# Kernel optimization log

Measured on AMD Instinct MI355X. Metric: run time of the kernel, lower is better.

The kernel has to match this reference:

```python
import jax, jax.numpy as jnp
import numpy as np

LATENT = 1024
ENC = 4096
B = 8192


def setup_inputs() -> dict:
    key = jax.random.key(0)
    k1, k2, k3, k4 = jax.random.split(key, 4)
    inp = jax.random.normal(k1, (B, LATENT), dtype=jnp.float32)
    enc = jax.random.normal(k2, (B, ENC), dtype=jnp.float32)
    # nn.Linear(ENC, LATENT): weight [LATENT, ENC], bias [LATENT]
    bound = 1.0 / np.sqrt(ENC)
    W = jax.random.uniform(k3, (LATENT, ENC), minval=-bound, maxval=bound, dtype=jnp.float32)
    b = jax.random.uniform(k4, (LATENT,), minval=-bound, maxval=bound, dtype=jnp.float32)
    return {"input": inp, "encoder_output": enc, "W": W, "b": b}


def reference(input, encoder_output, W, b):
    # vector = Linear(encoder_output)  -> [B, LATENT]
    v = jnp.einsum("be,de->bd", encoder_output, W) + b
    # Fused Householder-style reflection (math identical to bmm(vv^T, x)):
    # out = x - 2 * v * (v . x) / ||v||   (original divides by norm, not norm^2)
    dot = jnp.sum(v * input, axis=1, keepdims=True)          # [B, 1]
    norm = jnp.linalg.norm(v, axis=1, keepdims=True)         # [B, 1]
    output = input - 2.0 * v * dot / norm                    # [B, LATENT]
    log_det = jnp.zeros((input.shape[0], 1), dtype=input.dtype)
    return (output, log_det)
```

## Files before the change

### kernel.cpp

```cpp
#include <hip/hip_runtime.h>
#include <hip/hip_bf16.h>
#include <stdint.h>

#define M_DIM 8192
#define N_DIM 1024
#define K_DIM 4096

typedef __bf16 bf16x8 __attribute__((ext_vector_type(8)));
typedef float f32x4 __attribute__((ext_vector_type(4)));
typedef __hip_bfloat16 bf16_t;

__device__ __forceinline__ void gload_lds16(const void* g, void* l) {
  __builtin_amdgcn_global_load_lds(
      (const __attribute__((address_space(1))) void*)g,
      (__attribute__((address_space(3))) void*)l, 16, 0, 0);
}

__global__ __launch_bounds__(256) void pack_both(const float* __restrict__ enc,
                                                 const float* __restrict__ W,
                                                 int4* __restrict__ pA,
                                                 int4* __restrict__ pB) {
  const unsigned gtid = blockIdx.x * 256 + threadIdx.x;
  const float* src;
  int4* dst;
  unsigned t;
  if (gtid < 4194304u) { src = enc; dst = pA; t = gtid; }
  else                 { src = W;   dst = pB; t = gtid - 4194304u; }
  const unsigned cp = t & 7;
  const unsigned tmp = t >> 3;
  const unsigned r = tmp & 255;
  const unsigned tmp2 = tmp >> 8;
  const unsigned kt = tmp2 & 63;
  const unsigned rt = tmp2 >> 6;
  const unsigned srow = (rt << 8) + r;
  const unsigned k0 = (kt << 6) + ((cp ^ (r & 7)) << 3);
  const float4* s = (const float4*)(src + (size_t)srow * 4096 + k0);
  float4 a = s[0], b = s[1];
  union { bf16_t h[8]; int4 v; } u;
  u.h[0] = __float2bfloat16(a.x); u.h[1] = __float2bfloat16(a.y);
  u.h[2] = __float2bfloat16(a.z); u.h[3] = __float2bfloat16(a.w);
  u.h[4] = __float2bfloat16(b.x); u.h[5] = __float2bfloat16(b.y);
  u.h[6] = __float2bfloat16(b.z); u.h[7] = __float2bfloat16(b.w);
  dst[t] = u.v;
}

__device__ __forceinline__ void stage_half(const char* g, char* smem, int ldsoff, int tid) {
  gload_lds16(g + tid * 16, smem + ldsoff + tid * 16);
  gload_lds16(g + 8192 + tid * 16, smem + ldsoff + 8192 + tid * 16);
}

__global__ __launch_bounds__(512, 2) void gemm8(
    const char* __restrict__ pA, const char* __restrict__ pB,
    float* __restrict__ V0, float* __restrict__ V1p, int NT) {
  extern __shared__ char smem[];
  const int tid = threadIdx.x;
  const int lane = tid & 63, wave = tid >> 6;
  const int wm = wave >> 2, wn = wave & 3;
  const int lrow = lane & 15, lkc = lane >> 4;

  const int cpx = (int)gridDim.x >> 3;
  const int swz = ((int)blockIdx.x & 7) * cpx + ((int)blockIdx.x >> 3);
  const int split = swz >> 7;
  const int rem = swz & 127;
  const int mt = rem >> 2, nt = rem & 3;

  const char* Abase = pA + ((size_t)mt * 64 + (size_t)split * NT) * 32768;
  const char* Bbase = pB + ((size_t)nt * 64 + (size_t)split * NT) * 32768;
  float* V = split ? V1p : V0;

  int colw[2];
  colw[0] = ((lkc) ^ (lrow & 7)) << 4;
  colw[1] = ((4 + lkc) ^ (lrow & 7)) << 4;
  int aRow[4], bRow[2];
  #pragma unroll
  for (int f = 0; f < 4; ++f) aRow[f] = (wm * 64 + f * 16 + lrow) * 128;
  #pragma unroll
  for (int f2 = 0; f2 < 2; ++f2) bRow[f2] = 32768 + (wn * 32 + f2 * 16 + lrow) * 128;

  f32x4 acc[2][4][2][2];
  #pragma unroll
  for (int a0 = 0; a0 < 2; ++a0)
    #pragma unroll
    for (int a1 = 0; a1 < 4; ++a1)
      #pragma unroll
      for (int a2 = 0; a2 < 2; ++a2)
        #pragma unroll
        for (int a3 = 0; a3 < 2; ++a3)
          acc[a0][a1][a2][a3] = (f32x4){0.f, 0.f, 0.f, 0.f};

  const int ktm = NT - 1;

  stage_half(Abase,         smem, 0, tid);
  stage_half(Bbase,         smem, 32768, tid);
  stage_half(Bbase + 16384, smem, 49152, tid);
  stage_half(Abase + 16384, smem, 16384, tid);
  stage_half(Abase + 32768, smem, 65536, tid);
  asm volatile("s_waitcnt vmcnt(4)" ::: "memory");
  __builtin_amdgcn_sched_barrier(0);
  __builtin_amdgcn_s_barrier();

  bf16x8 aE[4][2], aO[4][2], b0[2][2], b1[2][2];
  #pragma unroll
  for (int f = 0; f < 4; ++f)
    #pragma unroll
    for (int s = 0; s < 2; ++s)
      aE[f][s] = *(const bf16x8*)(smem + aRow[f] + colw[s]);
  #pragma unroll
  for (int f2 = 0; f2 < 2; ++f2)
    #pragma unroll
    for (int s = 0; s < 2; ++s)
      b0[f2][s] = *(const bf16x8*)(smem + bRow[f2] + colw[s]);

  for (int g = 0; g < NT; ++g) {
    const int bb = g & 1, nbf = bb ^ 1;
    char* ab = smem + bb * 65536;
    char* nb = smem + nbf * 65536;
    const char* A1t = Abase + (size_t)((g + 1) & ktm) * 32768;
    const char* B1t = Bbase + (size_t)((g + 1) & ktm) * 32768;
    const char* A2t = Abase + (size_t)((g + 2) & ktm) * 32768;

    #pragma unroll
    for (int f2 = 0; f2 < 2; ++f2)
      #pragma unroll
      for (int s = 0; s < 2; ++s)
        b1[f2][s] = *(const bf16x8*)(ab + bRow[f2] + 16384 + colw[s]);
    stage_half(B1t, smem, nbf * 65536 + 32768, tid);
    stage_half(B1t + 16384, smem, nbf * 65536 + 49152, tid);
    __builtin_amdgcn_s_setprio(1);
    #pragma unroll
    for (int f = 0; f < 4; ++f)
      #pragma unroll
      for (int f2 = 0; f2 < 2; ++f2)
        #pragma unroll
        for (int s = 0; s < 2; ++s)
          acc[0][f][0][f2] = __builtin_amdgcn_mfma_f32_16x16x32_bf16(
              aE[f][s], b0[f2][s], acc[0][f][0][f2], 0, 0, 0);
    __builtin_amdgcn_s_setprio(0);
    asm volatile("s_waitcnt vmcnt(6)" ::: "memory");
    __builtin_amdgcn_sched_barrier(0);
    __builtin_amdgcn_s_barrier();

    #pragma unroll
    for (int f = 0; f < 4; ++f)
      #pragma unroll
      for (int s = 0; s < 2; ++s)
        aO[f][s] = *(const bf16x8*)(ab + aRow[f] + 16384 + colw[s]);
    stage_half(A1t + 16384, smem, nbf * 65536 + 16384, tid);
    __builtin_amdgcn_s_setprio(1);
    #pragma unroll
    for (int f = 0; f < 4; ++f)
      #pragma unroll
      for (int f2 = 0; f2 < 2; ++f2)
        #pragma unroll
        for (int s = 0; s < 2; ++s)
          acc[0][f][1][f2] = __builtin_amdgcn_mfma_f32_16x16x32_bf16(
              aE[f][s], b1[f2][s], acc[0][f][1][f2], 0, 0, 0);
    __builtin_amdgcn_s_setprio(0);
    __builtin_amdgcn_sched_barrier(0);
    __builtin_amdgcn_s_barrier();

    stage_half(A2t, smem, bb * 65536, tid);
    __builtin_amdgcn_s_setprio(1);
    #pragma unroll
    for (int f = 0; f < 4; ++f)
      #pragma unroll
      for (int f2 = 0; f2 < 2; ++f2)
        #pragma unroll
        for (int s = 0; s < 2; ++s)
          acc[1][f][1][f2] = __builtin_amdgcn_mfma_f32_16x16x32_bf16(
              aO[f][s], b1[f2][s], acc[1][f][1][f2], 0, 0, 0);
    __builtin_amdgcn_s_setprio(0);
    asm volatile("s_waitcnt vmcnt(8)" ::: "memory");
    __builtin_amdgcn_sched_barrier(0);
    __builtin_amdgcn_s_barrier();

    #pragma unroll
    for (int f = 0; f < 4; ++f)
      #pragma unroll
      for (int s = 0; s < 2; ++s)
        aE[f][s] = *(const bf16x8*)(nb + aRow[f] + colw[s]);
    __builtin_amdgcn_s_setprio(1);
    #pragma unroll
    for (int f = 0; f < 4; ++f)
      #pragma unroll
      for (int f2 = 0; f2 < 2; ++f2)
        #pragma unroll
        for (int s = 0; s < 2; ++s)
          acc[1][f][0][f2] = __builtin_amdgcn_mfma_f32_16x16x32_bf16(
              aO[f][s], b0[f2][s], acc[1][f][0][f2], 0, 0, 0);
    __builtin_amdgcn_s_setprio(0);
    __builtin_amdgcn_sched_barrier(0);
    asm volatile("s_waitcnt vmcnt(4)" ::: "memory");
    #pragma unroll
    for (int f2 = 0; f2 < 2; ++f2)
      #pragma unroll
      for (int s = 0; s < 2; ++s)
        b0[f2][s] = *(const bf16x8*)(nb + bRow[f2] + colw[s]);
    __builtin_amdgcn_sched_barrier(0);
    __builtin_amdgcn_s_barrier();
  }

  const int lq = lane >> 4;
  #pragma unroll
  for (int qm = 0; qm < 2; ++qm)
    #pragma unroll
    for (int f = 0; f < 4; ++f) {
      const int rowg = mt * 256 + qm * 128 + wm * 64 + f * 16 + lq * 4;
      #pragma unroll
      for (int reg = 0; reg < 4; ++reg) {
        float* Vr = V + (size_t)(rowg + reg) * N_DIM + nt * 256 + wn * 32 + lrow;
        #pragma unroll
        for (int qn = 0; qn < 2; ++qn)
          #pragma unroll
          for (int f2 = 0; f2 < 2; ++f2)
            Vr[qn * 128 + f2 * 16] = acc[qm][f][qn][f2][reg];
      }
    }
}

__global__ __launch_bounds__(256) void householder_ep(
    const float* __restrict__ x, const float* __restrict__ bias,
    float* __restrict__ vio, const float* __restrict__ V2,
    float* __restrict__ logdet) {
  const int row = blockIdx.x;
  const int t = threadIdx.x;
  float4* vr = (float4*)(vio + (size_t)row * N_DIM);
  const float4* xr = (const float4*)(x + (size_t)row * N_DIM);
  const float4* br = (const float4*)bias;

  float4 v = vr[t];
  if (V2) {
    float4 v2 = ((const float4*)(V2 + (size_t)row * N_DIM))[t];
    v.x += v2.x; v.y += v2.y; v.z += v2.z; v.w += v2.w;
  }
  float4 bb = br[t];
  v.x += bb.x; v.y += bb.y; v.z += bb.z; v.w += bb.w;
  float4 xx = xr[t];

  float dot = v.x * xx.x + v.y * xx.y + v.z * xx.z + v.w * xx.w;
  float nsq = v.x * v.x + v.y * v.y + v.z * v.z + v.w * v.w;

  #pragma unroll
  for (int off = 32; off > 0; off >>= 1) {
    dot += __shfl_down(dot, off);
    nsq += __shfl_down(nsq, off);
  }
  __shared__ float sd[4], sn[4];
  if ((t & 63) == 0) { sd[t >> 6] = dot; sn[t >> 6] = nsq; }
  __syncthreads();
  dot = sd[0] + sd[1] + sd[2] + sd[3];
  nsq = sn[0] + sn[1] + sn[2] + sn[3];

  const float f = 2.0f * dot / sqrtf(nsq);
  float4 o;
  o.x = xx.x - f * v.x;
  o.y = xx.y - f * v.y;
  o.z = xx.z - f * v.z;
  o.w = xx.w - f * v.w;
  vr[t] = o;
  if (t == 0) logdet[row] = 0.0f;
}

extern "C" void kernel_launch(void* const* d_in, const int* in_sizes, int n_in,
                              void* d_out, int out_size, void* d_ws, size_t ws_size,
                              hipStream_t stream) {
  const float* x   = (const float*)d_in[0];
  const float* enc = (const float*)d_in[1];
  const float* W   = (const float*)d_in[2];
  const float* b   = (const float*)d_in[3];

  float* out    = (float*)d_out;
  float* v      = out;
  float* logdet = out + (size_t)M_DIM * N_DIM;

  char*  packA = (char*)d_ws;
  char*  packB = packA + (size_t)64 * 1024 * 1024;
  float* V2    = (float*)(packB + (size_t)8 * 1024 * 1024);

  const size_t need2 = (size_t)104 * 1024 * 1024;
  const int nsplit = (ws_size >= need2) ? 2 : 1;

  pack_both<<<18432, 256, 0, stream>>>(enc, W, (int4*)packA, (int4*)packB);

  hipFuncSetAttribute((const void*)gemm8, hipFuncAttributeMaxDynamicSharedMemorySize, 131072);
  gemm8<<<dim3(128 * nsplit), 512, 131072, stream>>>(
      packA, packB, v, nsplit == 2 ? V2 : nullptr, 64 / nsplit);

  householder_ep<<<M_DIM, 256, 0, stream>>>(x, b, v, nsplit == 2 ? V2 : nullptr, logdet);
}
```

Baseline: 118.8 us.

## Store GEMM partials as bf16 and move LDS reads after MFMA blocks

The split-K GEMM partial results are now written to workspace as bf16 instead of fp32, and the epilogue reads and widens them. This halves the intermediate write and read traffic between the GEMM and the Householder epilogue, but rounding the partial sums to bf16 adds error to v. The LDS fragment loads for b1, aO and aE are also moved to after each MFMA group, before the barrier, so they overlap differently with matrix compute.

```diff
diff --git a/kernel.cpp b/kernel.cpp
--- a/kernel.cpp
+++ b/kernel.cpp
@@ -14,6 +14,12 @@
   __builtin_amdgcn_global_load_lds(
       (const __attribute__((address_space(1))) void*)g,
       (__attribute__((address_space(3))) void*)l, 16, 0, 0);
+}
+
+__device__ __forceinline__ float b2f(unsigned short u) {
+  union { unsigned i; float f; } x;
+  x.i = ((unsigned)u) << 16;
+  return x.f;
 }
 
 __global__ __launch_bounds__(256) void pack_both(const float* __restrict__ enc,
@@ -51,7 +57,7 @@
 
 __global__ __launch_bounds__(512, 2) void gemm8(
     const char* __restrict__ pA, const char* __restrict__ pB,
-    float* __restrict__ V0, float* __restrict__ V1p, int NT) {
+    bf16_t* __restrict__ V0, bf16_t* __restrict__ V1p, int NT) {
   extern __shared__ char smem[];
   const int tid = threadIdx.x;
   const int lane = tid & 63, wave = tid >> 6;
@@ -66,7 +72,7 @@
 
   const char* Abase = pA + ((size_t)mt * 64 + (size_t)split * NT) * 32768;
   const char* Bbase = pB + ((size_t)nt * 64 + (size_t)split * NT) * 32768;
-  float* V = split ? V1p : V0;
+  bf16_t* V = split ? V1p : V0;
 
   int colw[2];
   colw[0] = ((lkc) ^ (lrow & 7)) << 4;
@@ -119,11 +125,6 @@
     const char* B1t = Bbase + (size_t)((g + 1) & ktm) * 32768;
     const char* A2t = Abase + (size_t)((g + 2) & ktm) * 32768;
 
-    #pragma unroll
-    for (int f2 = 0; f2 < 2; ++f2)
-      #pragma unroll
-      for (int s = 0; s < 2; ++s)
-        b1[f2][s] = *(const bf16x8*)(ab + bRow[f2] + 16384 + colw[s]);
     stage_half(B1t, smem, nbf * 65536 + 32768, tid);
     stage_half(B1t + 16384, smem, nbf * 65536 + 49152, tid);
     __builtin_amdgcn_s_setprio(1);
@@ -136,15 +137,16 @@
           acc[0][f][0][f2] = __builtin_amdgcn_mfma_f32_16x16x32_bf16(
               aE[f][s], b0[f2][s], acc[0][f][0][f2], 0, 0, 0);
     __builtin_amdgcn_s_setprio(0);
+    __builtin_amdgcn_sched_barrier(0);
+    #pragma unroll
+    for (int f2 = 0; f2 < 2; ++f2)
+      #pragma unroll
+      for (int s = 0; s < 2; ++s)
+        b1[f2][s] = *(const bf16x8*)(ab + bRow[f2] + 16384 + colw[s]);
     asm volatile("s_waitcnt vmcnt(6)" ::: "memory");
     __builtin_amdgcn_sched_barrier(0);
     __builtin_amdgcn_s_barrier();
 
-    #pragma unroll
-    for (int f = 0; f < 4; ++f)
-      #pragma unroll
-      for (int s = 0; s < 2; ++s)
-        aO[f][s] = *(const bf16x8*)(ab + aRow[f] + 16384 + colw[s]);
     stage_half(A1t + 16384, smem, nbf * 65536 + 16384, tid);
     __builtin_amdgcn_s_setprio(1);
     #pragma unroll
@@ -157,6 +159,12 @@
               aE[f][s], b1[f2][s], acc[0][f][1][f2], 0, 0, 0);
     __builtin_amdgcn_s_setprio(0);
     __builtin_amdgcn_sched_barrier(0);
+    #pragma unroll
+    for (int f = 0; f < 4; ++f)
+      #pragma unroll
+      for (int s = 0; s < 2; ++s)
+        aO[f][s] = *(const bf16x8*)(ab + aRow[f] + 16384 + colw[s]);
+    __builtin_amdgcn_sched_barrier(0);
     __builtin_amdgcn_s_barrier();
 
     stage_half(A2t, smem, bb * 65536, tid);
@@ -170,15 +178,16 @@
           acc[1][f][1][f2] = __builtin_amdgcn_mfma_f32_16x16x32_bf16(
               aO[f][s], b1[f2][s], acc[1][f][1][f2], 0, 0, 0);
     __builtin_amdgcn_s_setprio(0);
+    __builtin_amdgcn_sched_barrier(0);
     asm volatile("s_waitcnt vmcnt(8)" ::: "memory");
-    __builtin_amdgcn_sched_barrier(0);
-    __builtin_amdgcn_s_barrier();
-
     #pragma unroll
     for (int f = 0; f < 4; ++f)
       #pragma unroll
       for (int s = 0; s < 2; ++s)
         aE[f][s] = *(const bf16x8*)(nb + aRow[f] + colw[s]);
+    __builtin_amdgcn_sched_barrier(0);
+    __builtin_amdgcn_s_barrier();
+
     __builtin_amdgcn_s_setprio(1);
     #pragma unroll
     for (int f = 0; f < 4; ++f)
@@ -208,30 +217,31 @@
       const int rowg = mt * 256 + qm * 128 + wm * 64 + f * 16 + lq * 4;
       #pragma unroll
       for (int reg = 0; reg < 4; ++reg) {
-        float* Vr = V + (size_t)(rowg + reg) * N_DIM + nt * 256 + wn * 32 + lrow;
+        bf16_t* Vr = V + (size_t)(rowg + reg) * N_DIM + nt * 256 + wn * 32 + lrow;
         #pragma unroll
         for (int qn = 0; qn < 2; ++qn)
           #pragma unroll
           for (int f2 = 0; f2 < 2; ++f2)
-            Vr[qn * 128 + f2 * 16] = acc[qm][f][qn][f2][reg];
+            Vr[qn * 128 + f2 * 16] = __float2bfloat16(acc[qm][f][qn][f2][reg]);
       }
     }
 }
 
 __global__ __launch_bounds__(256) void householder_ep(
     const float* __restrict__ x, const float* __restrict__ bias,
-    float* __restrict__ vio, const float* __restrict__ V2,
-    float* __restrict__ logdet) {
+    const unsigned short* __restrict__ V0b, const unsigned short* __restrict__ V1b,
+    float* __restrict__ out, float* __restrict__ logdet) {
   const int row = blockIdx.x;
   const int t = threadIdx.x;
-  float4* vr = (float4*)(vio + (size_t)row * N_DIM);
   const float4* xr = (const float4*)(x + (size_t)row * N_DIM);
   const float4* br = (const float4*)bias;
 
-  float4 v = vr[t];
-  if (V2) {
-    float4 v2 = ((const float4*)(V2 + (size_t)row * N_DIM))[t];
-    v.x += v2.x; v.y += v2.y; v.z += v2.z; v.w += v2.w;
+  ushort4 u0 = ((const ushort4*)(V0b + (size_t)row * N_DIM))[t];
+  float4 v;
+  v.x = b2f(u0.x); v.y = b2f(u0.y); v.z = b2f(u0.z); v.w = b2f(u0.w);
+  if (V1b) {
+    ushort4 u1 = ((const ushort4*)(V1b + (size_t)row * N_DIM))[t];
+    v.x += b2f(u1.x); v.y += b2f(u1.y); v.z += b2f(u1.z); v.w += b2f(u1.w);
   }
   float4 bb = br[t];
   v.x += bb.x; v.y += bb.y; v.z += bb.z; v.w += bb.w;
@@ -257,7 +267,7 @@
   o.y = xx.y - f * v.y;
   o.z = xx.z - f * v.z;
   o.w = xx.w - f * v.w;
-  vr[t] = o;
+  ((float4*)(out + (size_t)row * N_DIM))[t] = o;
   if (t == 0) logdet[row] = 0.0f;
 }
 
@@ -270,12 +280,12 @@
   const float* b   = (const float*)d_in[3];
 
   float* out    = (float*)d_out;
-  float* v      = out;
   float* logdet = out + (size_t)M_DIM * N_DIM;
 
-  char*  packA = (char*)d_ws;
-  char*  packB = packA + (size_t)64 * 1024 * 1024;
-  float* V2    = (float*)(packB + (size_t)8 * 1024 * 1024);
+  char*   packA = (char*)d_ws;
+  char*   packB = packA + (size_t)64 * 1024 * 1024;
+  bf16_t* V0b   = (bf16_t*)(packB + (size_t)8 * 1024 * 1024);
+  bf16_t* V1b   = V0b + (size_t)M_DIM * N_DIM;
 
   const size_t need2 = (size_t)104 * 1024 * 1024;
   const int nsplit = (ws_size >= need2) ? 2 : 1;
@@ -284,7 +294,9 @@
 
   hipFuncSetAttribute((const void*)gemm8, hipFuncAttributeMaxDynamicSharedMemorySize, 131072);
   gemm8<<<dim3(128 * nsplit), 512, 131072, stream>>>(
-      packA, packB, v, nsplit == 2 ? V2 : nullptr, 64 / nsplit);
-
-  householder_ep<<<M_DIM, 256, 0, stream>>>(x, b, v, nsplit == 2 ? V2 : nullptr, logdet);
-}
+      packA, packB, V0b, nsplit == 2 ? V1b : nullptr, 64 / nsplit);
+
+  householder_ep<<<M_DIM, 256, 0, stream>>>(
+      x, b, (const unsigned short*)V0b,
+      nsplit == 2 ? (const unsigned short*)V1b : nullptr, out, logdet);
+}
```

After: 116.2 us. -2.2%, faster.
